# Optimization experiments

Measured on AMD Instinct MI355X. Metric: run time of the kernel, lower is better.

The kernel has to match this reference:

```python
import jax, jax.numpy as jnp
import numpy as np

N_NODES = 100000
N_EDGES = 1600000
N_FEAT = 500
HID = 64
N_CLS = 40


def setup_inputs() -> dict:
    key = jax.random.key(0)
    ks = jax.random.split(key, 12)
    x = jax.random.normal(ks[0], (N_NODES, N_FEAT), dtype=jnp.float32)
    edge_index = jax.random.randint(ks[1], (2, N_EDGES), 0, N_NODES, dtype=jnp.int64)
    w_mul = jax.random.uniform(ks[2], (N_EDGES, 1), dtype=jnp.float32)
    s1 = 1.0 / np.sqrt(N_FEAT)
    s2 = 1.0 / np.sqrt(HID)
    # layer 1: lin(F->64), weight MLP: Linear(1,64,no bias)->LeakyReLU(0.2)->Linear(64,64,bias)
    w1 = jax.random.uniform(ks[3], (N_FEAT, HID), jnp.float32, -s1, s1)
    b1 = jax.random.uniform(ks[4], (HID,), jnp.float32, -s1, s1)
    m1a = jax.random.uniform(ks[5], (1, HID), jnp.float32, -1.0, 1.0)
    m1b_w = jax.random.uniform(ks[6], (HID, HID), jnp.float32, -s2, s2)
    m1b_b = jax.random.uniform(ks[7], (HID,), jnp.float32, -s2, s2)
    # layer 2: lin(64->C), weight MLP: Linear(1,C,no bias)->LeakyReLU(0.2)->Linear(C,C,bias)
    sc = 1.0 / np.sqrt(N_CLS)
    w2 = jax.random.uniform(ks[8], (HID, N_CLS), jnp.float32, -s2, s2)
    b2 = jax.random.uniform(ks[9], (N_CLS,), jnp.float32, -s2, s2)
    m2a = jax.random.uniform(ks[10], (1, N_CLS), jnp.float32, -1.0, 1.0)
    m2b_w = jax.random.uniform(ks[11], (N_CLS, N_CLS), jnp.float32, -sc, sc)
    m2b_b = jnp.zeros((N_CLS,), dtype=jnp.float32)
    return {"x": x, "edge_index": edge_index, "w_mul": w_mul,
            "w1": w1, "b1": b1, "m1a": m1a, "m1b_w": m1b_w, "m1b_b": m1b_b,
            "w2": w2, "b2": b2, "m2a": m2a, "m2b_w": m2b_w, "m2b_b": m2b_b}


def _segment_softmax(logits, seg, num_segments):
    # logits: [E, C], seg: [E]
    m = jax.ops.segment_max(logits, seg, num_segments=num_segments)
    m = jnp.where(jnp.isfinite(m), m, 0.0)
    e = jnp.exp(logits - m[seg])
    s = jax.ops.segment_sum(e, seg, num_segments=num_segments)
    return e / (s[seg] + 1e-16)


def _curvgn(x, edge_index, w_mul, lin_w, lin_b, ma, mb_w, mb_b, n_nodes):
    h = x @ lin_w + lin_b                                   # [N, C_out]
    ew = jax.nn.leaky_relu(w_mul @ ma, 0.2) @ mb_w + mb_b   # [E, C_out]
    ew = _segment_softmax(ew, edge_index[0], n_nodes)       # softmax over source groups (per CurvGN code)
    msg = ew * h[edge_index[0]]                             # [E, C_out]
    return jax.ops.segment_sum(msg, edge_index[1], num_segments=n_nodes)


def reference(x, edge_index, w_mul, w1, b1, m1a, m1b_w, m1b_b, w2, b2, m2a, m2b_w, m2b_b):
    n = x.shape[0]
    # dropout layers are identity in eval mode
    h = _curvgn(x, edge_index, w_mul, w1, b1, m1a, m1b_w, m1b_b, n)
    h = jax.nn.elu(h)
    h = _curvgn(h, edge_index, w_mul, w2, b2, m2a, m2b_w, m2b_b, n)
    return jax.nn.log_softmax(h, axis=1)
```

## Files before the change

kernel.cpp:

```cpp
#include <hip/hip_runtime.h>
#include <hip/hip_bf16.h>
#include <math.h>

#define NF 500
#define HID 64
#define NCLS 40
#define NBIN 256
#define KSTEPS 16
#define MAXB 8192
#define CAP 8192
#define AEPB 2048

typedef __attribute__((ext_vector_type(8))) short short8v;
typedef __attribute__((ext_vector_type(4))) float f32x4v;

__device__ inline short f2bf(float f) {
  unsigned u = __float_as_uint(f);
  unsigned r = u + 0x7fff + ((u >> 16) & 1);
  return (short)(r >> 16);
}
__device__ inline float bf2f(unsigned short u) {
  return __uint_as_float(((unsigned)u) << 16);
}
__device__ inline unsigned binof(int x, int rngb) {
  return (unsigned)x / (unsigned)rngb;
}


__global__ void prep_kernel(const float* __restrict__ m1a, const float* __restrict__ m1bw,
                            const float* __restrict__ m2a, const float* __restrict__ m2bw,
                            const float* __restrict__ w1,
                            float* __restrict__ c, short* __restrict__ wf) {
  if (blockIdx.x == 0) {
    int j = threadIdx.x;
    if (j < HID) {
      float sp = 0.f;
      for (int k = 0; k < HID; ++k) {
        float a = m1a[k];
        float ap = a > 0.f ? a : 0.2f * a;
        sp = fmaf(ap, m1bw[k * HID + j], sp);
      }
      c[j] = sp;
    }
    if (j < NCLS) {
      float sp = 0.f;
      for (int k = 0; k < NCLS; ++k) {
        float a = m2a[k];
        float ap = a > 0.f ? a : 0.2f * a;
        sp = fmaf(ap, m2bw[k * NCLS + j], sp);
      }
      c[128 + j] = sp;
    }
    return;
  }
  int idx = (blockIdx.x - 1) * 256 + threadIdx.x;
  if (idx >= KSTEPS * 4 * 64) return;
  int l = idx & 63;
  int f = (idx >> 6) & 3;
  int s = idx >> 8;
  int ch = f * 16 + (l & 15);
  int kb = s * 32 + (l >> 4) * 8;
  short8v v;
#pragma unroll
  for (int j = 0; j < 8; ++j) {
    int k = kb + j;
    v[j] = (k < NF) ? f2bf(w1[(size_t)k * HID + ch]) : (short)0;
  }
  ((short8v*)wf)[idx] = v;
}

__global__ __launch_bounds__(256, 4) void fused1_kernel(
    const int* __restrict__ ei, const float* __restrict__ wmul, int E, int rngb,
    int* __restrict__ binctl, long long* __restrict__ sbin, long long* __restrict__ dpair,
    int nbinA,
    const float* __restrict__ x, const short* __restrict__ wf,
    const float* __restrict__ b1, float* __restrict__ h1, int N) {
  const int tid = threadIdx.x;
  if ((int)blockIdx.x < nbinA) {
    __shared__ int cs[NBIN], cd[NBIN], bs[NBIN], bd[NBIN];
    cs[tid] = 0; cd[tid] = 0;
    __syncthreads();
    const int base = blockIdx.x * AEPB;
    int sv[8], dv[8], rs[8], rd[8];
    float tv[8];
#pragma unroll
    for (int u = 0; u < 8; ++u) {
      int e = base + u * 256 + tid;
      bool ok = e < E;
      sv[u] = ok ? __builtin_nontemporal_load(ei + e) : 0;
      dv[u] = ok ? __builtin_nontemporal_load(ei + E + e) : 0;
      tv[u] = ok ? __builtin_nontemporal_load(wmul + e) : 0.f;
      rs[u] = ok ? atomicAdd(&cs[binof(sv[u], rngb)], 1) : 0;
      rd[u] = ok ? atomicAdd(&cd[binof(dv[u], rngb)], 1) : 0;
    }
    __syncthreads();
    bs[tid] = tid * CAP + (cs[tid] ? atomicAdd(&binctl[512 + tid], cs[tid]) : 0);
    bd[tid] = tid * CAP + (cd[tid] ? atomicAdd(&binctl[768 + tid], cd[tid]) : 0);
    __syncthreads();
#pragma unroll
    for (int u = 0; u < 8; ++u) {
      int e = base + u * 256 + tid;
      if (e < E) {
        unsigned ks = binof(sv[u], rngb);
        unsigned kd = binof(dv[u], rngb);
        unsigned tb = (unsigned)__float_as_uint(tv[u]);
        sbin[bs[ks] + rs[u]] =
            (long long)(((unsigned long long)tb << 32) | (unsigned)sv[u]);
        unsigned dloc = (unsigned)dv[u] - kd * (unsigned)rngb;
        unsigned lo = (unsigned)sv[u] | (dloc << 17);
        dpair[bd[kd] + rd[u]] =
            (long long)(((unsigned long long)tb << 32) | lo);
      }
    }
    return;
  }
  const int gb = blockIdx.x - nbinA;
  const int wv = tid >> 6, l = tid & 63;
  const int lr = l & 15, lk = l >> 4;
  const int n0 = gb * 128 + wv * 32;
  int r0 = n0 + lr, r1 = r0 + 16;
  const float* p0 = x + (size_t)min(r0, N - 1) * NF + lk * 8;
  const float* p1 = x + (size_t)min(r1, N - 1) * NF + lk * 8;
  const short8v* wfv = (const short8v*)wf;

  f32x4v acc[2][4];
#pragma unroll
  for (int mi = 0; mi < 2; ++mi)
#pragma unroll
    for (int f = 0; f < 4; ++f) acc[mi][f] = (f32x4v){0.f, 0.f, 0.f, 0.f};

  const float4 z4 = make_float4(0.f, 0.f, 0.f, 0.f);
#pragma unroll
  for (int s = 0; s < KSTEPS; ++s) {
    float4 a0l, a0h, a1l, a1h;
    if (s < KSTEPS - 1) {
      a0l = *(const float4*)(p0 + s * 32);
      a0h = *(const float4*)(p0 + s * 32 + 4);
      a1l = *(const float4*)(p1 + s * 32);
      a1h = *(const float4*)(p1 + s * 32 + 4);
    } else {
      int k = (KSTEPS - 1) * 32 + lk * 8;
      if (k + 8 <= NF) {
        a0l = *(const float4*)(p0 + s * 32);
        a0h = *(const float4*)(p0 + s * 32 + 4);
        a1l = *(const float4*)(p1 + s * 32);
        a1h = *(const float4*)(p1 + s * 32 + 4);
      } else if (k + 4 <= NF) {
        a0l = *(const float4*)(p0 + s * 32); a0h = z4;
        a1l = *(const float4*)(p1 + s * 32); a1h = z4;
      } else {
        a0l = a0h = a1l = a1h = z4;
      }
    }
    short8v b[4];
#pragma unroll
    for (int f = 0; f < 4; ++f) b[f] = wfv[(s * 4 + f) * 64 + l];
    short8v a0, a1;
    a0[0] = f2bf(a0l.x); a0[1] = f2bf(a0l.y); a0[2] = f2bf(a0l.z); a0[3] = f2bf(a0l.w);
    a0[4] = f2bf(a0h.x); a0[5] = f2bf(a0h.y); a0[6] = f2bf(a0h.z); a0[7] = f2bf(a0h.w);
    a1[0] = f2bf(a1l.x); a1[1] = f2bf(a1l.y); a1[2] = f2bf(a1l.z); a1[3] = f2bf(a1l.w);
    a1[4] = f2bf(a1h.x); a1[5] = f2bf(a1h.y); a1[6] = f2bf(a1h.z); a1[7] = f2bf(a1h.w);
#pragma unroll
    for (int f = 0; f < 4; ++f) {
      acc[0][f] = __builtin_amdgcn_mfma_f32_16x16x32_bf16(a0, b[f], acc[0][f], 0, 0, 0);
      acc[1][f] = __builtin_amdgcn_mfma_f32_16x16x32_bf16(a1, b[f], acc[1][f], 0, 0, 0);
    }
  }

#pragma unroll
  for (int mi = 0; mi < 2; ++mi) {
    int nbase = n0 + mi * 16 + lk * 4;
#pragma unroll
    for (int f = 0; f < 4; ++f) {
      int ch = f * 16 + lr;
      float bb = b1[ch];
#pragma unroll
      for (int reg = 0; reg < 4; ++reg) {
        int nd = nbase + reg;
        if (nd < N) h1[(size_t)nd * HID + ch] = acc[mi][f][reg] + bb;
      }
    }
  }
}

__global__ __launch_bounds__(256) void binscan_kernel(int* __restrict__ binctl) {
  __shared__ int ws[4];
  const int tid = threadIdx.x, lane = tid & 63, wv = tid >> 6;
  for (int seg = 0; seg < 2; ++seg) {
    int v = binctl[512 + seg * 256 + tid];
    int x = v;
#pragma unroll
    for (int off = 1; off < 64; off <<= 1) {
      int y = __shfl_up(x, off);
      if (lane >= off) x += y;
    }
    if (lane == 63) ws[wv] = x;
    __syncthreads();
    int woff = 0;
    for (int k = 0; k < wv; ++k) woff += ws[k];
    int excl = woff + x - v;
    binctl[1024 + seg * 257 + tid] = excl;
    if (tid == 255) binctl[1024 + seg * 257 + 256] = excl + v;
    __syncthreads();
  }
}

__global__ __launch_bounds__(256) void scatter4_kernel(const int* __restrict__ binctl,
    const long long* __restrict__ sbin, const long long* __restrict__ dpair,
    int* __restrict__ off_src, int* __restrict__ off_dst,
    float* __restrict__ t_src, long long* __restrict__ pair, int N, int rngb) {
  __shared__ long long stg[MAXB];
  __shared__ int deg[400], loc[400];
  __shared__ int wsum[4];
  const int i = blockIdx.x;
  const int tid = threadIdx.x;
  const bool isrc = i < NBIN;
  const int p = isrc ? i : i - NBIN;
  const int nbase = p * rngb;
  const int nn = min(rngb, N - nbase);
  const int rbase = p * CAP;
  int cnt, obase;
  if (isrc) { cnt = binctl[512 + p]; obase = binctl[1024 + p]; }
  else      { cnt = binctl[768 + p]; obase = binctl[1281 + p]; }
  const int rend = rbase + cnt;
  for (int k = tid; k < nn; k += 256) deg[k] = 0;
  __syncthreads();
  if (isrc) {
    for (int idx = rbase + tid; idx < rend; idx += 256) {
      int s = (int)(unsigned)(sbin[idx] & 0xffffffffLL);
      atomicAdd(&deg[s - nbase], 1);
    }
  } else {
    for (int idx = rbase + tid; idx < rend; idx += 256) {
      unsigned lo = (unsigned)(dpair[idx] & 0xffffffffLL);
      atomicAdd(&deg[(lo >> 17) & 0x1FF], 1);
    }
  }
  __syncthreads();
  const int k0 = 2 * tid, k1 = 2 * tid + 1;
  const int v0 = (k0 < nn) ? deg[k0] : 0;
  const int v1 = (k1 < nn) ? deg[k1] : 0;
  const int ts = v0 + v1;
  const int lane = tid & 63, wv = tid >> 6;
  int x = ts;
#pragma unroll
  for (int o = 1; o < 64; o <<= 1) {
    int y = __shfl_up(x, o);
    if (lane >= o) x += y;
  }
  if (lane == 63) wsum[wv] = x;
  __syncthreads();
  int woff = 0;
  for (int k = 0; k < wv; ++k) woff += wsum[k];
  const int excl = woff + x - ts;
  if (k0 < nn) loc[k0] = excl;
  if (k1 < nn) loc[k1] = excl + v0;
  __syncthreads();
  int* off = isrc ? off_src : off_dst;
  for (int k = tid; k < nn; k += 256) off[nbase + k] = obase + loc[k];
  if (tid == 0) {
    if (i == NBIN - 1) off_src[N] = binctl[1024 + NBIN];
    if (i == 2 * NBIN - 1) off_dst[N] = binctl[1281 + NBIN];
  }
  __syncthreads();
  if (isrc) {
    float* stf = (float*)stg;
    for (int idx = rbase + tid; idx < rend; idx += 256) {
      long long pk = sbin[idx];
      int s = (int)(unsigned)(pk & 0xffffffffLL);
      float t = __uint_as_float((unsigned)((unsigned long long)pk >> 32));
      int lpos = atomicAdd(&loc[s - nbase], 1);
      if (lpos < 2 * MAXB) stf[lpos] = t;
      else t_src[obase + lpos] = t;
    }
    __syncthreads();
    const int c2 = min(cnt, 2 * MAXB);
    for (int k = tid; k < c2; k += 256) t_src[obase + k] = stf[k];
  } else {
    for (int idx = rbase + tid; idx < rend; idx += 256) {
      long long pk = dpair[idx];
      unsigned lo = (unsigned)(pk & 0xffffffffLL);
      int dloc = (lo >> 17) & 0x1FF;
      long long clean = (long long)((pk & 0xffffffff00000000LL) |
                                    (unsigned long long)(lo & 0x1FFFFu));
      int lpos = atomicAdd(&loc[dloc], 1);
      if (lpos < MAXB) stg[lpos] = clean;
      else pair[obase + lpos] = clean;
    }
    __syncthreads();
    const int c2 = min(cnt, MAXB);
    for (int k = tid; k < c2; k += 256) pair[obase + k] = stg[k];
  }
}

__global__ void dpass_kernel(const int* __restrict__ off_src, const float* __restrict__ t_src,
                             const float* __restrict__ c, const float* __restrict__ h1,
                             unsigned short* __restrict__ g1b,
                             float* __restrict__ invD2, int N) {
  int node = blockIdx.x * 4 + (threadIdx.x >> 6);
  if (node >= N) return;
  int lane = threadIdx.x & 63;
  float c1p = c[lane];
  float c2p = lane < NCLS ? c[128 + lane] : 0.f;
  int b = off_src[node], e = off_src[node + 1];
  float d1 = 0.f, d2 = 0.f;
  for (int i = b; i < e; ++i) {
    float t = t_src[i];
    d1 += __expf(t * c1p);
    d2 += __expf(t * c2p);
  }
  float h = h1[(size_t)node * HID + lane];
  g1b[(size_t)node * HID + lane] = (unsigned short)f2bf(d1 > 0.f ? h / d1 : 0.f);
  if (lane < NCLS) invD2[(size_t)node * NCLS + lane] = d2 > 0.f ? 1.f / d2 : 0.f;
}

__global__ __launch_bounds__(256) void aggB_kernel(const int* __restrict__ off_dst,
    const long long* __restrict__ pair, const float* __restrict__ c,
    const unsigned short* __restrict__ g1b, const float* __restrict__ w2,
    const float* __restrict__ b2, const float* __restrict__ invD2,
    unsigned short* __restrict__ g2p, int N) {
  __shared__ float sw2[HID * NCLS];
  __shared__ float sb2[NCLS];
  __shared__ float sa[4][72];
  const int tid = threadIdx.x;
  for (int i = tid; i < HID * NCLS; i += 256) sw2[i] = w2[i];
  if (tid < NCLS) sb2[tid] = b2[tid];
  const int w = tid >> 6;
  const int node = blockIdx.x * 4 + w;
  const bool valid = node < N;
  const int l = tid & 63;
  const int u = l >> 3;
  const int q = l & 7;
  float c1p8[8];
#pragma unroll
  for (int j = 0; j < 8; ++j) c1p8[j] = c[q * 8 + j];
  const int b = valid ? off_dst[node] : 0;
  const int e = valid ? off_dst[node + 1] : 0;
  float acc8[8] = {};
  for (int i = b; i < e; i += 16) {
    int idx0 = i + u, idx1 = i + 8 + u;
    bool ok0 = idx0 < e, ok1 = idx1 < e;
    long long pk0 = pair[ok0 ? idx0 : b];
    long long pk1 = pair[ok1 ? idx1 : b];
    int s0 = (int)(unsigned)(pk0 & 0xffffffffLL);
    int s1 = (int)(unsigned)(pk1 & 0xffffffffLL);
    float t0 = __uint_as_float((unsigned)((unsigned long long)pk0 >> 32));
    float t1 = __uint_as_float((unsigned)((unsigned long long)pk1 >> 32));
    short8v gv0 = *(const short8v*)(g1b + ((size_t)s0 << 6) + (q << 3));
    short8v gv1 = *(const short8v*)(g1b + ((size_t)s1 << 6) + (q << 3));
#pragma unroll
    for (int j = 0; j < 8; ++j) {
      float f0 = ok0 ? __expf(t0 * c1p8[j]) : 0.f;
      float f1 = ok1 ? __expf(t1 * c1p8[j]) : 0.f;
      acc8[j] = fmaf(f0, bf2f((unsigned short)gv0[j]), acc8[j]);
      acc8[j] = fmaf(f1, bf2f((unsigned short)gv1[j]), acc8[j]);
    }
  }
#pragma unroll
  for (int j = 0; j < 8; ++j) {
    acc8[j] += __shfl_xor(acc8[j], 8);
    acc8[j] += __shfl_xor(acc8[j], 16);
    acc8[j] += __shfl_xor(acc8[j], 32);
  }
  if (u == 0) {
#pragma unroll
    for (int j = 0; j < 8; ++j) {
      float v = acc8[j];
      sa[w][q * 8 + j] = v > 0.f ? v : __expf(v) - 1.f;
    }
  }
  __syncthreads();
  if (valid) {
    if (l < NCLS) {
      float acc = 0.f;
#pragma unroll
      for (int k = 0; k < HID; ++k) acc = fmaf(sa[w][k], sw2[k * NCLS + l], acc);
      g2p[(size_t)node * 64 + l] =
          (unsigned short)f2bf((acc + sb2[l]) * invD2[(size_t)node * NCLS + l]);
    } else {
      g2p[(size_t)node * 64 + l] = 0;
    }
  }
}

__global__ __launch_bounds__(256) void aggC_kernel(const int* __restrict__ off_dst,
    const long long* __restrict__ pair, const float* __restrict__ c,
    const unsigned short* __restrict__ g2p, float* __restrict__ out, int N) {
  int node = blockIdx.x * 4 + (threadIdx.x >> 6);
  if (node >= N) return;
  const int l = threadIdx.x & 63;
  const int u = l >> 3;
  const int q = l & 7;
  float c2p8[8];
#pragma unroll
  for (int j = 0; j < 8; ++j) {
    int ch = q * 8 + j;
    c2p8[j] = (ch < NCLS) ? c[128 + ch] : 0.f;
  }
  const int b = off_dst[node], e = off_dst[node + 1];
  float acc8[8] = {};
  for (int i = b; i < e; i += 16) {
    int idx0 = i + u, idx1 = i + 8 + u;
    bool ok0 = idx0 < e, ok1 = idx1 < e;
    long long pk0 = pair[ok0 ? idx0 : b];
    long long pk1 = pair[ok1 ? idx1 : b];
    int s0 = (int)(unsigned)(pk0 & 0xffffffffLL);
    int s1 = (int)(unsigned)(pk1 & 0xffffffffLL);
    float t0 = __uint_as_float((unsigned)((unsigned long long)pk0 >> 32));
    float t1 = __uint_as_float((unsigned)((unsigned long long)pk1 >> 32));
    short8v gv0 = *(const short8v*)(g2p + ((size_t)s0 << 6) + (q << 3));
    short8v gv1 = *(const short8v*)(g2p + ((size_t)s1 << 6) + (q << 3));
#pragma unroll
    for (int j = 0; j < 8; ++j) {
      float f0 = ok0 ? __expf(t0 * c2p8[j]) : 0.f;
      float f1 = ok1 ? __expf(t1 * c2p8[j]) : 0.f;
      acc8[j] = fmaf(f0, bf2f((unsigned short)gv0[j]), acc8[j]);
      acc8[j] = fmaf(f1, bf2f((unsigned short)gv1[j]), acc8[j]);
    }
  }
#pragma unroll
  for (int j = 0; j < 8; ++j) {
    acc8[j] += __shfl_xor(acc8[j], 8);
    acc8[j] += __shfl_xor(acc8[j], 16);
    acc8[j] += __shfl_xor(acc8[j], 32);
  }
  float m = -INFINITY;
#pragma unroll
  for (int j = 0; j < 8; ++j) {
    if (q * 8 + j < NCLS) m = fmaxf(m, acc8[j]);
  }
  m = fmaxf(m, __shfl_xor(m, 1));
  m = fmaxf(m, __shfl_xor(m, 2));
  m = fmaxf(m, __shfl_xor(m, 4));
  float ssum = 0.f;
#pragma unroll
  for (int j = 0; j < 8; ++j) {
    if (q * 8 + j < NCLS) ssum += __expf(acc8[j] - m);
  }
  ssum += __shfl_xor(ssum, 1);
  ssum += __shfl_xor(ssum, 2);
  ssum += __shfl_xor(ssum, 4);
  float ls = __logf(ssum);
  if (u == 0 && q < 5) {
#pragma unroll
    for (int j = 0; j < 8; ++j)
      out[(size_t)node * NCLS + q * 8 + j] = acc8[j] - m - ls;
  }
}

extern "C" void kernel_launch(void* const* d_in, const int* in_sizes, int n_in,
                              void* d_out, int out_size, void* d_ws, size_t ws_size,
                              hipStream_t stream) {
  const float* x    = (const float*)d_in[0];
  const int*   ei   = (const int*)d_in[1];
  const float* wmul = (const float*)d_in[2];
  const float* w1   = (const float*)d_in[3];
  const float* b1   = (const float*)d_in[4];
  const float* m1a  = (const float*)d_in[5];
  const float* m1bw = (const float*)d_in[6];
  const float* w2   = (const float*)d_in[8];
  const float* b2   = (const float*)d_in[9];
  const float* m2a  = (const float*)d_in[10];
  const float* m2bw = (const float*)d_in[11];
  float* out = (float*)d_out;

  const int N = in_sizes[0] / NF;
  const int E = in_sizes[2];

  char* ws = (char*)d_ws;
  size_t off = 0;
  auto carve = [&](size_t bytes) -> void* {
    void* p = ws + off;
    off = (off + bytes + 255) & ~(size_t)255;
    return p;
  };
  int*   off_src = (int*)carve((size_t)2 * (N + 1) * sizeof(int));
  int*   off_dst = off_src + (N + 1);
  float* cvec    = (float*)carve(208 * sizeof(float));
  int*   binctl  = (int*)carve(1600 * sizeof(int));
  short* wf      = (short*)carve((size_t)KSTEPS * 4 * 64 * 8 * sizeof(short));
  float* t_src   = (float*)carve((size_t)E * sizeof(float));
  long long* pair = (long long*)carve((size_t)E * sizeof(long long));
  char*  binmem  = (char*)carve((size_t)2 * NBIN * CAP * 8);
  long long* sbin  = (long long*)binmem;
  long long* dpair = (long long*)(binmem + (size_t)NBIN * CAP * 8);
  float* h1      = (float*)carve((size_t)N * HID * sizeof(float));
  float* invD2   = (float*)carve((size_t)N * NCLS * sizeof(float));
  unsigned short* g1b = (unsigned short*)carve((size_t)N * HID * sizeof(unsigned short));
  unsigned short* g2p = (unsigned short*)binmem;

  const int rngb  = (N + NBIN - 1) / NBIN;
  const int nbinA = (E + AEPB - 1) / AEPB;
  const int ngemm = (N + 127) / 128;

  hipMemsetAsync(binctl, 0, 1600 * sizeof(int), stream);
  prep_kernel<<<17, 256, 0, stream>>>(m1a, m1bw, m2a, m2bw, w1, cvec, wf);
  fused1_kernel<<<nbinA + ngemm, 256, 0, stream>>>(ei, wmul, E, rngb, binctl,
                                                   sbin, dpair, nbinA,
                                                   x, wf, b1, h1, N);
  binscan_kernel<<<1, 256, 0, stream>>>(binctl);
  scatter4_kernel<<<2 * NBIN, 256, 0, stream>>>(binctl, sbin, dpair,
                                                off_src, off_dst, t_src, pair, N, rngb);
  dpass_kernel<<<(N + 3) / 4, 256, 0, stream>>>(off_src, t_src, cvec, h1, g1b, invD2, N);
  aggB_kernel<<<(N + 3) / 4, 256, 0, stream>>>(off_dst, pair, cvec, g1b, w2, b2,
                                               invD2, g2p, N);
  aggC_kernel<<<(N + 3) / 4, 256, 0, stream>>>(off_dst, pair, cvec, g2p, out, N);
}
```

Measured before the change: 360.1 us.

## Split fused bin/GEMM kernel and alias h1 into freed bin scratch

```diff
diff --git a/kernel.cpp b/kernel.cpp
--- a/kernel.cpp
+++ b/kernel.cpp
@@ -69,55 +69,164 @@
   ((short8v*)wf)[idx] = v;
 }
 
-__global__ __launch_bounds__(256, 4) void fused1_kernel(
-    const int* __restrict__ ei, const float* __restrict__ wmul, int E, int rngb,
-    int* __restrict__ binctl, long long* __restrict__ sbin, long long* __restrict__ dpair,
-    int nbinA,
-    const float* __restrict__ x, const short* __restrict__ wf,
-    const float* __restrict__ b1, float* __restrict__ h1, int N) {
+__global__ __launch_bounds__(256) void binA_kernel(const int* __restrict__ ei,
+    const float* __restrict__ wmul, int E, int rngb, int* __restrict__ binctl,
+    long long* __restrict__ sbin, long long* __restrict__ dpair) {
+  __shared__ int cs[NBIN], cd[NBIN], bs[NBIN], bd[NBIN];
   const int tid = threadIdx.x;
-  if ((int)blockIdx.x < nbinA) {
-    __shared__ int cs[NBIN], cd[NBIN], bs[NBIN], bd[NBIN];
-    cs[tid] = 0; cd[tid] = 0;
+  cs[tid] = 0; cd[tid] = 0;
+  __syncthreads();
+  const int base = blockIdx.x * AEPB;
+  int sv[8], dv[8], rs[8], rd[8];
+  float tv[8];
+#pragma unroll
+  for (int u = 0; u < 8; ++u) {
+    int e = base + u * 256 + tid;
+    bool ok = e < E;
+    sv[u] = ok ? __builtin_nontemporal_load(ei + e) : 0;
+    dv[u] = ok ? __builtin_nontemporal_load(ei + E + e) : 0;
+    tv[u] = ok ? __builtin_nontemporal_load(wmul + e) : 0.f;
+    rs[u] = ok ? atomicAdd(&cs[binof(sv[u], rngb)], 1) : 0;
+    rd[u] = ok ? atomicAdd(&cd[binof(dv[u], rngb)], 1) : 0;
+  }
+  __syncthreads();
+  bs[tid] = tid * CAP + (cs[tid] ? atomicAdd(&binctl[512 + tid], cs[tid]) : 0);
+  bd[tid] = tid * CAP + (cd[tid] ? atomicAdd(&binctl[768 + tid], cd[tid]) : 0);
+  __syncthreads();
+#pragma unroll
+  for (int u = 0; u < 8; ++u) {
+    int e = base + u * 256 + tid;
+    if (e < E) {
+      unsigned ks = binof(sv[u], rngb);
+      unsigned kd = binof(dv[u], rngb);
+      unsigned tb = (unsigned)__float_as_uint(tv[u]);
+      sbin[bs[ks] + rs[u]] =
+          (long long)(((unsigned long long)tb << 32) | (unsigned)sv[u]);
+      unsigned dloc = (unsigned)dv[u] - kd * (unsigned)rngb;
+      unsigned lo = (unsigned)sv[u] | (dloc << 17);
+      dpair[bd[kd] + rd[u]] =
+          (long long)(((unsigned long long)tb << 32) | lo);
+    }
+  }
+}
+
+__global__ __launch_bounds__(256) void binscan_kernel(int* __restrict__ binctl) {
+  __shared__ int ws[4];
+  const int tid = threadIdx.x, lane = tid & 63, wv = tid >> 6;
+  for (int seg = 0; seg < 2; ++seg) {
+    int v = binctl[512 + seg * 256 + tid];
+    int x = v;
+#pragma unroll
+    for (int off = 1; off < 64; off <<= 1) {
+      int y = __shfl_up(x, off);
+      if (lane >= off) x += y;
+    }
+    if (lane == 63) ws[wv] = x;
     __syncthreads();
-    const int base = blockIdx.x * AEPB;
-    int sv[8], dv[8], rs[8], rd[8];
-    float tv[8];
-#pragma unroll
-    for (int u = 0; u < 8; ++u) {
-      int e = base + u * 256 + tid;
-      bool ok = e < E;
-      sv[u] = ok ? __builtin_nontemporal_load(ei + e) : 0;
-      dv[u] = ok ? __builtin_nontemporal_load(ei + E + e) : 0;
-      tv[u] = ok ? __builtin_nontemporal_load(wmul + e) : 0.f;
-      rs[u] = ok ? atomicAdd(&cs[binof(sv[u], rngb)], 1) : 0;
-      rd[u] = ok ? atomicAdd(&cd[binof(dv[u], rngb)], 1) : 0;
-    }
+    int woff = 0;
+    for (int k = 0; k < wv; ++k) woff += ws[k];
+    int excl = woff + x - v;
+    binctl[1024 + seg * 257 + tid] = excl;
+    if (tid == 255) binctl[1024 + seg * 257 + 256] = excl + v;
     __syncthreads();
-    bs[tid] = tid * CAP + (cs[tid] ? atomicAdd(&binctl[512 + tid], cs[tid]) : 0);
-    bd[tid] = tid * CAP + (cd[tid] ? atomicAdd(&binctl[768 + tid], cd[tid]) : 0);
+  }
+}
+
+__global__ __launch_bounds__(256) void scatter4_kernel(const int* __restrict__ binctl,
+    const long long* __restrict__ sbin, const long long* __restrict__ dpair,
+    int* __restrict__ off_src, int* __restrict__ off_dst,
+    float* __restrict__ t_src, long long* __restrict__ pair, int N, int rngb) {
+  __shared__ long long stg[MAXB];
+  __shared__ int deg[400], loc[400];
+  __shared__ int wsum[4];
+  const int i = blockIdx.x;
+  const int tid = threadIdx.x;
+  const bool isrc = i < NBIN;
+  const int p = isrc ? i : i - NBIN;
+  const int nbase = p * rngb;
+  const int nn = min(rngb, N - nbase);
+  const int rbase = p * CAP;
+  int cnt, obase;
+  if (isrc) { cnt = binctl[512 + p]; obase = binctl[1024 + p]; }
+  else      { cnt = binctl[768 + p]; obase = binctl[1281 + p]; }
+  const int rend = rbase + cnt;
+  for (int k = tid; k < nn; k += 256) deg[k] = 0;
+  __syncthreads();
+  if (isrc) {
+    for (int idx = rbase + tid; idx < rend; idx += 256) {
+      int s = (int)(unsigned)(sbin[idx] & 0xffffffffLL);
+      atomicAdd(&deg[s - nbase], 1);
+    }
+  } else {
+    for (int idx = rbase + tid; idx < rend; idx += 256) {
+      unsigned lo = (unsigned)(dpair[idx] & 0xffffffffLL);
+      atomicAdd(&deg[(lo >> 17) & 0x1FF], 1);
+    }
+  }
+  __syncthreads();
+  const int k0 = 2 * tid, k1 = 2 * tid + 1;
+  const int v0 = (k0 < nn) ? deg[k0] : 0;
+  const int v1 = (k1 < nn) ? deg[k1] : 0;
+  const int ts = v0 + v1;
+  const int lane = tid & 63, wv = tid >> 6;
+  int x = ts;
+#pragma unroll
+  for (int o = 1; o < 64; o <<= 1) {
+    int y = __shfl_up(x, o);
+    if (lane >= o) x += y;
+  }
+  if (lane == 63) wsum[wv] = x;
+  __syncthreads();
+  int woff = 0;
+  for (int k = 0; k < wv; ++k) woff += wsum[k];
+  const int excl = woff + x - ts;
+  if (k0 < nn) loc[k0] = excl;
+  if (k1 < nn) loc[k1] = excl + v0;
+  __syncthreads();
+  int* off = isrc ? off_src : off_dst;
+  for (int k = tid; k < nn; k += 256) off[nbase + k] = obase + loc[k];
+  if (tid == 0) {
+    if (i == NBIN - 1) off_src[N] = binctl[1024 + NBIN];
+    if (i == 2 * NBIN - 1) off_dst[N] = binctl[1281 + NBIN];
+  }
+  __syncthreads();
+  if (isrc) {
+    float* stf = (float*)stg;
+    for (int idx = rbase + tid; idx < rend; idx += 256) {
+      long long pk = sbin[idx];
+      int s = (int)(unsigned)(pk & 0xffffffffLL);
+      float t = __uint_as_float((unsigned)((unsigned long long)pk >> 32));
+      int lpos = atomicAdd(&loc[s - nbase], 1);
+      if (lpos < 2 * MAXB) stf[lpos] = t;
+      else t_src[obase + lpos] = t;
+    }
     __syncthreads();
-#pragma unroll
-    for (int u = 0; u < 8; ++u) {
-      int e = base + u * 256 + tid;
-      if (e < E) {
-        unsigned ks = binof(sv[u], rngb);
-        unsigned kd = binof(dv[u], rngb);
-        unsigned tb = (unsigned)__float_as_uint(tv[u]);
-        sbin[bs[ks] + rs[u]] =
-            (long long)(((unsigned long long)tb << 32) | (unsigned)sv[u]);
-        unsigned dloc = (unsigned)dv[u] - kd * (unsigned)rngb;
-        unsigned lo = (unsigned)sv[u] | (dloc << 17);
-        dpair[bd[kd] + rd[u]] =
-            (long long)(((unsigned long long)tb << 32) | lo);
-      }
-    }
-    return;
-  }
-  const int gb = blockIdx.x - nbinA;
+    const int c2 = min(cnt, 2 * MAXB);
+    for (int k = tid; k < c2; k += 256) t_src[obase + k] = stf[k];
+  } else {
+    for (int idx = rbase + tid; idx < rend; idx += 256) {
+      long long pk = dpair[idx];
+      unsigned lo = (unsigned)(pk & 0xffffffffLL);
+      int dloc = (lo >> 17) & 0x1FF;
+      long long clean = (long long)((pk & 0xffffffff00000000LL) |
+                                    (unsigned long long)(lo & 0x1FFFFu));
+      int lpos = atomicAdd(&loc[dloc], 1);
+      if (lpos < MAXB) stg[lpos] = clean;
+      else pair[obase + lpos] = clean;
+    }
+    __syncthreads();
+    const int c2 = min(cnt, MAXB);
+    for (int k = tid; k < c2; k += 256) pair[obase + k] = stg[k];
+  }
+}
+
+__global__ __launch_bounds__(256, 4) void gemm1_mfma(const float* __restrict__ x,
+    const short* __restrict__ wf, const float* __restrict__ b1,
+    float* __restrict__ h1, int N) {
+  const int tid = threadIdx.x;
   const int wv = tid >> 6, l = tid & 63;
   const int lr = l & 15, lk = l >> 4;
-  const int n0 = gb * 128 + wv * 32;
+  const int n0 = blockIdx.x * 128 + wv * 32;
   int r0 = n0 + lr, r1 = r0 + 16;
   const float* p0 = x + (size_t)min(r0, N - 1) * NF + lk * 8;
   const float* p1 = x + (size_t)min(r1, N - 1) * NF + lk * 8;
@@ -183,116 +292,6 @@
   }
 }
 
-__global__ __launch_bounds__(256) void binscan_kernel(int* __restrict__ binctl) {
-  __shared__ int ws[4];
-  const int tid = threadIdx.x, lane = tid & 63, wv = tid >> 6;
-  for (int seg = 0; seg < 2; ++seg) {
-    int v = binctl[512 + seg * 256 + tid];
-    int x = v;
-#pragma unroll
-    for (int off = 1; off < 64; off <<= 1) {
-      int y = __shfl_up(x, off);
-      if (lane >= off) x += y;
-    }
-    if (lane == 63) ws[wv] = x;
-    __syncthreads();
-    int woff = 0;
-    for (int k = 0; k < wv; ++k) woff += ws[k];
-    int excl = woff + x - v;
-    binctl[1024 + seg * 257 + tid] = excl;
-    if (tid == 255) binctl[1024 + seg * 257 + 256] = excl + v;
-    __syncthreads();
-  }
-}
-
-__global__ __launch_bounds__(256) void scatter4_kernel(const int* __restrict__ binctl,
-    const long long* __restrict__ sbin, const long long* __restrict__ dpair,
-    int* __restrict__ off_src, int* __restrict__ off_dst,
-    float* __restrict__ t_src, long long* __restrict__ pair, int N, int rngb) {
-  __shared__ long long stg[MAXB];
-  __shared__ int deg[400], loc[400];
-  __shared__ int wsum[4];
-  const int i = blockIdx.x;
-  const int tid = threadIdx.x;
-  const bool isrc = i < NBIN;
-  const int p = isrc ? i : i - NBIN;
-  const int nbase = p * rngb;
-  const int nn = min(rngb, N - nbase);
-  const int rbase = p * CAP;
-  int cnt, obase;
-  if (isrc) { cnt = binctl[512 + p]; obase = binctl[1024 + p]; }
-  else      { cnt = binctl[768 + p]; obase = binctl[1281 + p]; }
-  const int rend = rbase + cnt;
-  for (int k = tid; k < nn; k += 256) deg[k] = 0;
-  __syncthreads();
-  if (isrc) {
-    for (int idx = rbase + tid; idx < rend; idx += 256) {
-      int s = (int)(unsigned)(sbin[idx] & 0xffffffffLL);
-      atomicAdd(&deg[s - nbase], 1);
-    }
-  } else {
-    for (int idx = rbase + tid; idx < rend; idx += 256) {
-      unsigned lo = (unsigned)(dpair[idx] & 0xffffffffLL);
-      atomicAdd(&deg[(lo >> 17) & 0x1FF], 1);
-    }
-  }
-  __syncthreads();
-  const int k0 = 2 * tid, k1 = 2 * tid + 1;
-  const int v0 = (k0 < nn) ? deg[k0] : 0;
-  const int v1 = (k1 < nn) ? deg[k1] : 0;
-  const int ts = v0 + v1;
-  const int lane = tid & 63, wv = tid >> 6;
-  int x = ts;
-#pragma unroll
-  for (int o = 1; o < 64; o <<= 1) {
-    int y = __shfl_up(x, o);
-    if (lane >= o) x += y;
-  }
-  if (lane == 63) wsum[wv] = x;
-  __syncthreads();
-  int woff = 0;
-  for (int k = 0; k < wv; ++k) woff += wsum[k];
-  const int excl = woff + x - ts;
-  if (k0 < nn) loc[k0] = excl;
-  if (k1 < nn) loc[k1] = excl + v0;
-  __syncthreads();
-  int* off = isrc ? off_src : off_dst;
-  for (int k = tid; k < nn; k += 256) off[nbase + k] = obase + loc[k];
-  if (tid == 0) {
-    if (i == NBIN - 1) off_src[N] = binctl[1024 + NBIN];
-    if (i == 2 * NBIN - 1) off_dst[N] = binctl[1281 + NBIN];
-  }
-  __syncthreads();
-  if (isrc) {
-    float* stf = (float*)stg;
-    for (int idx = rbase + tid; idx < rend; idx += 256) {
-      long long pk = sbin[idx];
-      int s = (int)(unsigned)(pk & 0xffffffffLL);
-      float t = __uint_as_float((unsigned)((unsigned long long)pk >> 32));
-      int lpos = atomicAdd(&loc[s - nbase], 1);
-      if (lpos < 2 * MAXB) stf[lpos] = t;
-      else t_src[obase + lpos] = t;
-    }
-    __syncthreads();
-    const int c2 = min(cnt, 2 * MAXB);
-    for (int k = tid; k < c2; k += 256) t_src[obase + k] = stf[k];
-  } else {
-    for (int idx = rbase + tid; idx < rend; idx += 256) {
-      long long pk = dpair[idx];
-      unsigned lo = (unsigned)(pk & 0xffffffffLL);
-      int dloc = (lo >> 17) & 0x1FF;
-      long long clean = (long long)((pk & 0xffffffff00000000LL) |
-                                    (unsigned long long)(lo & 0x1FFFFu));
-      int lpos = atomicAdd(&loc[dloc], 1);
-      if (lpos < MAXB) stg[lpos] = clean;
-      else pair[obase + lpos] = clean;
-    }
-    __syncthreads();
-    const int c2 = min(cnt, MAXB);
-    for (int k = tid; k < c2; k += 256) pair[obase + k] = stg[k];
-  }
-}
-
 __global__ void dpass_kernel(const int* __restrict__ off_src, const float* __restrict__ t_src,
                              const float* __restrict__ c, const float* __restrict__ h1,
                              unsigned short* __restrict__ g1b,
@@ -484,23 +483,21 @@
   char*  binmem  = (char*)carve((size_t)2 * NBIN * CAP * 8);
   long long* sbin  = (long long*)binmem;
   long long* dpair = (long long*)(binmem + (size_t)NBIN * CAP * 8);
-  float* h1      = (float*)carve((size_t)N * HID * sizeof(float));
+  float* h1      = (float*)binmem;
   float* invD2   = (float*)carve((size_t)N * NCLS * sizeof(float));
   unsigned short* g1b = (unsigned short*)carve((size_t)N * HID * sizeof(unsigned short));
-  unsigned short* g2p = (unsigned short*)binmem;
-
-  const int rngb  = (N + NBIN - 1) / NBIN;
-  const int nbinA = (E + AEPB - 1) / AEPB;
-  const int ngemm = (N + 127) / 128;
+  unsigned short* g2p = (unsigned short*)(binmem + (size_t)NBIN * CAP * 8);
+
+  const int rngb = (N + NBIN - 1) / NBIN;
 
   hipMemsetAsync(binctl, 0, 1600 * sizeof(int), stream);
   prep_kernel<<<17, 256, 0, stream>>>(m1a, m1bw, m2a, m2bw, w1, cvec, wf);
-  fused1_kernel<<<nbinA + ngemm, 256, 0, stream>>>(ei, wmul, E, rngb, binctl,
-                                                   sbin, dpair, nbinA,
-                                                   x, wf, b1, h1, N);
+  binA_kernel<<<(E + AEPB - 1) / AEPB, 256, 0, stream>>>(ei, wmul, E, rngb, binctl,
+                                                         sbin, dpair);
   binscan_kernel<<<1, 256, 0, stream>>>(binctl);
   scatter4_kernel<<<2 * NBIN, 256, 0, stream>>>(binctl, sbin, dpair,
                                                 off_src, off_dst, t_src, pair, N, rngb);
+  gemm1_mfma<<<(N + 127) / 128, 256, 0, stream>>>(x, wf, b1, h1, N);
   dpass_kernel<<<(N + 3) / 4, 256, 0, stream>>>(off_src, t_src, cvec, h1, g1b, invD2, N);
   aggB_kernel<<<(N + 3) / 4, 256, 0, stream>>>(off_dst, pair, cvec, g1b, w2, b2,
                                                invD2, g2p, N);
```

Measured after the change: 355.1 us. Within noise of the previous version (-1.4%).
